# Optimization experiments

Hardware: AMD Instinct MI355X
Metric: run time of the kernel (lower is better)

Reference implementation:

```python
import jax, jax.numpy as jnp
import numpy as np

KS = 7            # kernel_size
DIL = 1           # dilatation
H = 96
W = 96
PAD = DIL * (KS - 1) // 2
SHIFTS = [s * DIL for s in range(KS)]


def stack_kernel(a, axis=-2):
    # a: [B, H+2*PAD, W+2*PAD, C] -> [B, H, W, ks^2, C] (or stacked on `axis`)
    return jnp.stack([a[:, y:H + y, x:W + x] for y in SHIFTS for x in SHIFTS], axis=axis)


def make_padding_mask():
    # zeros inside, -inf in the halo; stacked per window position -> [1,H,W,ks^2]
    z = jnp.pad(jnp.zeros((1, H, W, 1), jnp.float32),
                ((0, 0), (PAD, PAD), (PAD, PAD), (0, 0)),
                constant_values=-jnp.inf)
    return stack_kernel(z, axis=-1)[..., 0, :]  # [1,H,W,ks^2]


def setup_inputs() -> dict:
    key = jax.random.key(0)
    ks = jax.random.split(key, 8)
    B, C, KD, OD = 2, 128, 64, 128
    Q = jax.random.normal(ks[0], (B, H, W, C), jnp.float32)
    K = jax.random.normal(ks[1], (B, H, W, C), jnp.float32)
    V = jax.random.normal(ks[2], (B, H, W, C), jnp.float32)
    s = 1.0 / np.sqrt(C)
    Wq = jax.random.normal(ks[3], (C, KD), jnp.float32) * s
    Wk = jax.random.normal(ks[4], (C, KD), jnp.float32) * s
    Wv = jax.random.normal(ks[5], (C, OD), jnp.float32) * s
    return {"Q": Q, "K": K, "V": V,
            "Wq": Wq, "bq": jnp.zeros((KD,), jnp.float32),
            "Wk": Wk, "bk": jnp.zeros((KD,), jnp.float32),
            "Wv": Wv, "bv": jnp.zeros((OD,), jnp.float32)}


def reference(Q, K, V, Wq, bq, Wk, bk, Wv, bv):
    # Dense projections (key_dim is not None)
    q = Q @ Wq + bq                      # [B,H,W,KD]
    k = K @ Wk + bk                      # [B,H,W,KD]
    Dk = jnp.asarray(q.shape[-1], q.dtype)

    pad4 = ((0, 0), (PAD, PAD), (PAD, PAD), (0, 0))
    k_stk = stack_kernel(jnp.pad(k, pad4), axis=-2)   # [B,H,W,ks^2,KD]
    mask = make_padding_mask()                        # [1,H,W,ks^2]

    # w = Q . K_neighbors + padding mask; softmax over ks^2 window
    w = jnp.einsum('bhwd,bhwkd->bhwk', q, k_stk) + mask
    scores = jax.nn.softmax(w / jnp.sqrt(Dk), axis=-1)  # [B,H,W,ks^2]

    v_stk = stack_kernel(jnp.pad(V, pad4), axis=-2)   # [B,H,W,ks^2,E]
    out = jnp.einsum('bhwk,bhwke->bhwe', scores, v_stk)
    # V_d Dense with relu (out_dim is not None)
    out = jax.nn.relu(out @ Wv + bv)                  # [B,H,W,out_dim]
    return out
```

## Files before the change

### kernel.cpp

```cpp
#include <hip/hip_runtime.h>
#include <math.h>

#define BH 2
#define HH 96
#define WW 96
#define CC 128
#define NPIX (BH*HH*WW)

#define TH 8
#define TW 4
#define NH 140
#define NHP 160

#define NEGBIG (-3.0e38f)

typedef __attribute__((ext_vector_type(8))) short short8;
typedef __attribute__((ext_vector_type(4))) float f32x4;

__device__ __forceinline__ unsigned short f2bf(float f) {
    union { float f; unsigned u; } a; a.f = f;
    return (unsigned short)((a.u + 0x7FFFu + ((a.u >> 16) & 1u)) >> 16);
}
__device__ __forceinline__ unsigned packbf(float x, float y) {
    return (unsigned)f2bf(x) | ((unsigned)f2bf(y) << 16);
}

__global__ __launch_bounds__(256) void prep_proj_kernel(
    const float* __restrict__ Qg, const float* __restrict__ Kg,
    const float* __restrict__ V,  const float* __restrict__ Wq,
    const float* __restrict__ bq, const float* __restrict__ Wk,
    const float* __restrict__ bk, const float* __restrict__ Wv,
    unsigned short* __restrict__ q_bf, unsigned short* __restrict__ k_bf,
    unsigned short* __restrict__ v_bf, unsigned short* __restrict__ WvT)
{
    const int bid = blockIdx.x;
    const int tid = threadIdx.x;

    if (bid < 576) {
        const int lane = tid & 63;
        const int wvv  = tid >> 6;
        const int gw   = bid * 4 + wvv;
        const bool isq = gw < 1152;
        const int row0 = (isq ? gw : gw - 1152) * 16;

        const float* __restrict__ X   = isq ? Qg : Kg;
        const float* __restrict__ Wt  = isq ? Wq : Wk;
        const float* __restrict__ bia = isq ? bq : bk;
        unsigned short* __restrict__ Y = isq ? q_bf : k_bf;

        const int qd = lane >> 4, m = lane & 15;

        short8 afr[4];
        #pragma unroll
        for (int ks = 0; ks < 4; ++ks) {
            const float4* __restrict__ src = reinterpret_cast<const float4*>(
                X + (size_t)(row0 + m) * 128 + ks * 32 + qd * 8);
            const float4 a0 = src[0], a1 = src[1];
            short8 f;
            f[0] = (short)f2bf(a0.x); f[1] = (short)f2bf(a0.y);
            f[2] = (short)f2bf(a0.z); f[3] = (short)f2bf(a0.w);
            f[4] = (short)f2bf(a1.x); f[5] = (short)f2bf(a1.y);
            f[6] = (short)f2bf(a1.z); f[7] = (short)f2bf(a1.w);
            afr[ks] = f;
        }

        #pragma unroll
        for (int n = 0; n < 4; ++n) {
            f32x4 acc = {};
            #pragma unroll
            for (int ks = 0; ks < 4; ++ks) {
                short8 bfr;
                #pragma unroll
                for (int j = 0; j < 8; ++j)
                    bfr[j] = (short)f2bf(Wt[(ks * 32 + qd * 8 + j) * 64 + n * 16 + m]);
                acc = __builtin_amdgcn_mfma_f32_16x16x32_bf16(afr[ks], bfr, acc, 0, 0, 0);
            }
            const int col = n * 16 + m;
            const float bb = bia[col];
            #pragma unroll
            for (int r = 0; r < 4; ++r)
                Y[(size_t)(row0 + qd * 4 + r) * 64 + col] = f2bf(acc[r] + bb);
        }
    } else if (bid < 1728) {
        const int idx = (bid - 576) * 256 + tid;
        const float4* __restrict__ V4 = reinterpret_cast<const float4*>(V);
        const float4 a = V4[idx * 2], b = V4[idx * 2 + 1];
        uint4 o;
        o.x = packbf(a.x, a.y); o.y = packbf(a.z, a.w);
        o.z = packbf(b.x, b.y); o.w = packbf(b.z, b.w);
        reinterpret_cast<uint4*>(v_bf)[idx] = o;
    } else {
        const int base = (bid - 1728) * 1024 + tid * 4;
        #pragma unroll
        for (int i = 0; i < 4; ++i) {
            const int e = base + i;
            WvT[e] = f2bf(Wv[(e & 127) * 128 + (e >> 7)]);
        }
    }
}

#define PS_OFF 0
#define PS_STRIDE 168
#define AS_OFF 5376
#define AS_STRIDE 136
#define SM_OFF 9728
#define OFF_OFF 9984
#define LDS_N 10304

__global__ __launch_bounds__(256) void attn_kernel(
    const unsigned short* __restrict__ q_bf, const unsigned short* __restrict__ k_bf,
    const unsigned short* __restrict__ v_bf, const unsigned short* __restrict__ WvT,
    const float* __restrict__ bv, float* __restrict__ out)
{
    __shared__ unsigned short lds[LDS_N];
    const int tid  = threadIdx.x;
    const int lane = tid & 63;
    const int wv   = tid >> 6;
    const int mt   = wv & 1;
    const int ng   = wv >> 1;

    const int bid  = blockIdx.x;
    const int bimg = bid / 288;
    const int tidx = bid % 288;
    const int ty = tidx / 24, tx = tidx % 24;
    const int y0 = ty * TH, x0 = tx * TW;

    const int qd = lane >> 4, m = lane & 15;

    int* __restrict__ offsI = reinterpret_cast<int*>(&lds[OFF_OFF]);
    float* __restrict__ smf = reinterpret_cast<float*>(&lds[SM_OFF]);

    if (tid < NHP) {
        const int r = tid;
        const int hy = (r * 6554) >> 16;
        const int hx = r - hy * 10;
        const int iy = y0 - 3 + hy, ix = x0 - 3 + hx;
        int o = -1;
        if (((unsigned)iy < HH) & ((unsigned)ix < WW) & (r < NH))
            o = (bimg * HH + iy) * WW + ix;
        offsI[r] = o;
    }
    __syncthreads();

    short8 qa[2];
    {
        const int p  = mt * 16 + m;
        const int py = p >> 2, px = p & 3;
        const size_t gq = (size_t)(bimg * HH + y0 + py) * WW + (x0 + px);
        #pragma unroll
        for (int ks = 0; ks < 2; ++ks)
            qa[ks] = *reinterpret_cast<const short8*>(q_bf + gq * 64 + ks * 32 + qd * 8);
    }

    f32x4 sc[5];
    int offh[5];
    #pragma unroll
    for (int n5 = 0; n5 < 5; ++n5) {
        const int nt = ng * 5 + n5;
        const int oh = offsI[nt * 16 + m];
        offh[n5] = oh;
        const size_t ob = (size_t)(oh < 0 ? 0 : oh) * 64;
        f32x4 a = {};
        #pragma unroll
        for (int ks = 0; ks < 2; ++ks) {
            const short8 bfr = *reinterpret_cast<const short8*>(k_bf + ob + ks * 32 + qd * 8);
            a = __builtin_amdgcn_mfma_f32_16x16x32_bf16(qa[ks], bfr, a, 0, 0, 0);
        }
        sc[n5] = a;
    }

    float mx[4] = {NEGBIG, NEGBIG, NEGBIG, NEGBIG};
    #pragma unroll
    for (int n5 = 0; n5 < 5; ++n5) {
        const int h  = (ng * 5 + n5) * 16 + m;
        const int hy = (h * 6554) >> 16;
        const int hx = h - hy * 10;
        const bool imgok = offh[n5] >= 0;
        #pragma unroll
        for (int r = 0; r < 4; ++r) {
            const int p  = mt * 16 + qd * 4 + r;
            const int py = p >> 2, px = p & 3;
            const bool ok = imgok & ((unsigned)(hy - py) <= 6u) & ((unsigned)(hx - px) <= 6u);
            const float s = ok ? sc[n5][r] * 0.125f : NEGBIG;
            sc[n5][r] = s;
            mx[r] = fmaxf(mx[r], s);
        }
    }
    #pragma unroll
    for (int r = 0; r < 4; ++r)
        #pragma unroll
        for (int off = 1; off < 16; off <<= 1)
            mx[r] = fmaxf(mx[r], __shfl_xor(mx[r], off));

    float sm[4] = {0.f, 0.f, 0.f, 0.f};
    #pragma unroll
    for (int n5 = 0; n5 < 5; ++n5)
        #pragma unroll
        for (int r = 0; r < 4; ++r) {
            const float s = sc[n5][r];
            const float e = (s > -1.0e38f) ? __expf(s - mx[r]) : 0.f;
            sc[n5][r] = e;
            sm[r] += e;
        }
    #pragma unroll
    for (int r = 0; r < 4; ++r)
        #pragma unroll
        for (int off = 1; off < 16; off <<= 1)
            sm[r] += __shfl_xor(sm[r], off);

    if (m == 0) {
        #pragma unroll
        for (int r = 0; r < 4; ++r) {
            const int row = mt * 16 + qd * 4 + r;
            smf[row * 2 + ng]      = mx[r];
            smf[64 + row * 2 + ng] = sm[r];
        }
    }
    __syncthreads();

    float fac[4];
    #pragma unroll
    for (int r = 0; r < 4; ++r) {
        const int row = mt * 16 + qd * 4 + r;
        const float m0 = smf[row * 2 + 0];
        const float m1 = smf[row * 2 + 1];
        const float M  = fmaxf(m0, m1);
        const float s0 = smf[64 + row * 2 + 0];
        const float s1 = smf[64 + row * 2 + 1];
        const float S  = s0 * __expf(m0 - M) + s1 * __expf(m1 - M);
        fac[r] = __expf(mx[r] - M) / S;
    }

    #pragma unroll
    for (int n5 = 0; n5 < 5; ++n5)
        #pragma unroll
        for (int r = 0; r < 4; ++r) {
            const int row = mt * 16 + qd * 4 + r;
            const int col = (ng * 5 + n5) * 16 + m;
            lds[PS_OFF + row * PS_STRIDE + col] = f2bf(sc[n5][r] * fac[r]);
        }
    __syncthreads();

    short8 pa[5];
    #pragma unroll
    for (int ks = 0; ks < 5; ++ks)
        pa[ks] = *reinterpret_cast<const short8*>(
            &lds[PS_OFF + (mt * 16 + m) * PS_STRIDE + ks * 32 + qd * 8]);

    f32x4 oacc[4] = {};
    #pragma unroll
    for (int ks = 0; ks < 5; ++ks) {
        const unsigned short* vbase[8];
        #pragma unroll
        for (int j = 0; j < 8; ++j) {
            const int o = offsI[ks * 32 + qd * 8 + j];
            vbase[j] = v_bf + (size_t)(o < 0 ? 0 : o) * 128;
        }
        #pragma unroll
        for (int n4 = 0; n4 < 4; ++n4) {
            const int ch = (ng * 4 + n4) * 16 + m;
            short8 bfr;
            #pragma unroll
            for (int j = 0; j < 8; ++j)
                bfr[j] = (short)vbase[j][ch];
            oacc[n4] = __builtin_amdgcn_mfma_f32_16x16x32_bf16(pa[ks], bfr, oacc[n4], 0, 0, 0);
        }
    }

    #pragma unroll
    for (int n4 = 0; n4 < 4; ++n4)
        #pragma unroll
        for (int r = 0; r < 4; ++r) {
            const int row = mt * 16 + qd * 4 + r;
            const int col = (ng * 4 + n4) * 16 + m;
            lds[AS_OFF + row * AS_STRIDE + col] = f2bf(oacc[n4][r]);
        }
    __syncthreads();

    short8 aa[4];
    #pragma unroll
    for (int ks = 0; ks < 4; ++ks)
        aa[ks] = *reinterpret_cast<const short8*>(
            &lds[AS_OFF + (mt * 16 + m) * AS_STRIDE + ks * 32 + qd * 8]);

    #pragma unroll
    for (int n4 = 0; n4 < 4; ++n4) {
        const int nt = ng * 4 + n4;
        f32x4 a = {};
        #pragma unroll
        for (int ks = 0; ks < 4; ++ks) {
            const short8 bfr = *reinterpret_cast<const short8*>(
                WvT + (nt * 16 + m) * 128 + ks * 32 + qd * 8);
            a = __builtin_amdgcn_mfma_f32_16x16x32_bf16(aa[ks], bfr, a, 0, 0, 0);
        }
        const int col = nt * 16 + m;
        const float bb = bv[col];
        #pragma unroll
        for (int r = 0; r < 4; ++r) {
            const int p  = mt * 16 + qd * 4 + r;
            const int py = p >> 2, px = p & 3;
            const size_t gp = (size_t)(bimg * HH + y0 + py) * WW + (x0 + px);
            out[gp * 128 + col] = fmaxf(a[r] + bb, 0.f);
        }
    }
}

extern "C" void kernel_launch(void* const* d_in, const int* in_sizes, int n_in,
                              void* d_out, int out_size, void* d_ws, size_t ws_size,
                              hipStream_t stream)
{
    const float* Q  = (const float*)d_in[0];
    const float* K  = (const float*)d_in[1];
    const float* V  = (const float*)d_in[2];
    const float* Wq = (const float*)d_in[3];
    const float* bq = (const float*)d_in[4];
    const float* Wk = (const float*)d_in[5];
    const float* bk = (const float*)d_in[6];
    const float* Wv = (const float*)d_in[7];
    const float* bv = (const float*)d_in[8];
    float* out = (float*)d_out;

    unsigned short* WvT  = (unsigned short*)d_ws;
    unsigned short* q_bf = WvT + 16384;
    unsigned short* k_bf = q_bf + (size_t)NPIX * 64;
    unsigned short* v_bf = k_bf + (size_t)NPIX * 64;

    prep_proj_kernel<<<1744, 256, 0, stream>>>(Q, K, V, Wq, bq, Wk, bk, Wv,
                                               q_bf, k_bf, v_bf, WvT);
    attn_kernel<<<576, 256, 0, stream>>>(q_bf, k_bf, v_bf, WvT, bv, out);
}
```

Measured before the change: 110.8 us.

## Stage V halo in LDS from fp32, pre-transpose weights, drop V bf16 pass

Removes the separate V-to-bf16 conversion pass. The attention kernel now loads the fp32 V halo tile straight from global memory into LDS, converting and swizzling it there, so the PV MFMA operands are gathered from LDS instead of scattered global loads. Weight transposition to bf16 moves into a small kernel so the projection kernel does vector loads of pre-transposed weights. Each wave also computes all ten score tiles itself, which removes the cross-wave softmax reduction and one barrier at the price of duplicated QK MFMAs. The trade-offs are an extra kernel launch and larger LDS use, which may lower occupancy.

```diff
diff --git a/kernel.cpp b/kernel.cpp
--- a/kernel.cpp
+++ b/kernel.cpp
@@ -4,7 +4,6 @@
 #define BH 2
 #define HH 96
 #define WW 96
-#define CC 128
 #define NPIX (BH*HH*WW)
 
 #define TH 8
@@ -25,91 +24,79 @@
     return (unsigned)f2bf(x) | ((unsigned)f2bf(y) << 16);
 }
 
-__global__ __launch_bounds__(256) void prep_proj_kernel(
+__global__ __launch_bounds__(256) void wprep_kernel(
+    const float* __restrict__ Wq, const float* __restrict__ Wk,
+    const float* __restrict__ Wv, unsigned short* __restrict__ wbase)
+{
+    const int e = blockIdx.x * 256 + threadIdx.x;
+    if (e < 8192)       { wbase[e] = f2bf(Wq[(e & 127) * 64 + (e >> 7)]); }
+    else if (e < 16384) { const int t = e - 8192;
+                          wbase[e] = f2bf(Wk[(t & 127) * 64 + (t >> 7)]); }
+    else                { const int t = e - 16384;
+                          wbase[e] = f2bf(Wv[(t & 127) * 128 + (t >> 7)]); }
+}
+
+__global__ __launch_bounds__(256) void proj_kernel(
     const float* __restrict__ Qg, const float* __restrict__ Kg,
-    const float* __restrict__ V,  const float* __restrict__ Wq,
-    const float* __restrict__ bq, const float* __restrict__ Wk,
-    const float* __restrict__ bk, const float* __restrict__ Wv,
-    unsigned short* __restrict__ q_bf, unsigned short* __restrict__ k_bf,
-    unsigned short* __restrict__ v_bf, unsigned short* __restrict__ WvT)
-{
-    const int bid = blockIdx.x;
-    const int tid = threadIdx.x;
-
-    if (bid < 576) {
-        const int lane = tid & 63;
-        const int wvv  = tid >> 6;
-        const int gw   = bid * 4 + wvv;
-        const bool isq = gw < 1152;
-        const int row0 = (isq ? gw : gw - 1152) * 16;
-
-        const float* __restrict__ X   = isq ? Qg : Kg;
-        const float* __restrict__ Wt  = isq ? Wq : Wk;
-        const float* __restrict__ bia = isq ? bq : bk;
-        unsigned short* __restrict__ Y = isq ? q_bf : k_bf;
-
-        const int qd = lane >> 4, m = lane & 15;
-
-        short8 afr[4];
+    const unsigned short* __restrict__ wbase,
+    const float* __restrict__ bq, const float* __restrict__ bk,
+    unsigned short* __restrict__ q_bf, unsigned short* __restrict__ k_bf)
+{
+    const int tid  = threadIdx.x;
+    const int lane = tid & 63;
+    const int wvv  = tid >> 6;
+    const int gw   = blockIdx.x * 4 + wvv;
+    const bool isq = gw < 1152;
+    const int row0 = (isq ? gw : gw - 1152) * 16;
+
+    const float* __restrict__ X = isq ? Qg : Kg;
+    const unsigned short* __restrict__ WT = isq ? wbase : (wbase + 8192);
+    const float* __restrict__ bia = isq ? bq : bk;
+    unsigned short* __restrict__ Y = isq ? q_bf : k_bf;
+
+    const int qd = lane >> 4, m = lane & 15;
+
+    short8 afr[4];
+    #pragma unroll
+    for (int ks = 0; ks < 4; ++ks) {
+        const float4* __restrict__ src = reinterpret_cast<const float4*>(
+            X + (size_t)(row0 + m) * 128 + ks * 32 + qd * 8);
+        const float4 a0 = src[0], a1 = src[1];
+        short8 f;
+        f[0] = (short)f2bf(a0.x); f[1] = (short)f2bf(a0.y);
+        f[2] = (short)f2bf(a0.z); f[3] = (short)f2bf(a0.w);
+        f[4] = (short)f2bf(a1.x); f[5] = (short)f2bf(a1.y);
+        f[6] = (short)f2bf(a1.z); f[7] = (short)f2bf(a1.w);
+        afr[ks] = f;
+    }
+
+    #pragma unroll
+    for (int n = 0; n < 4; ++n) {
+        f32x4 acc = {};
         #pragma unroll
         for (int ks = 0; ks < 4; ++ks) {
-            const float4* __restrict__ src = reinterpret_cast<const float4*>(
-                X + (size_t)(row0 + m) * 128 + ks * 32 + qd * 8);
-            const float4 a0 = src[0], a1 = src[1];
-            short8 f;
-            f[0] = (short)f2bf(a0.x); f[1] = (short)f2bf(a0.y);
-            f[2] = (short)f2bf(a0.z); f[3] = (short)f2bf(a0.w);
-            f[4] = (short)f2bf(a1.x); f[5] = (short)f2bf(a1.y);
-            f[6] = (short)f2bf(a1.z); f[7] = (short)f2bf(a1.w);
-            afr[ks] = f;
-        }
-
-        #pragma unroll
-        for (int n = 0; n < 4; ++n) {
-            f32x4 acc = {};
-            #pragma unroll
-            for (int ks = 0; ks < 4; ++ks) {
-                short8 bfr;
-                #pragma unroll
-                for (int j = 0; j < 8; ++j)
-                    bfr[j] = (short)f2bf(Wt[(ks * 32 + qd * 8 + j) * 64 + n * 16 + m]);
-                acc = __builtin_amdgcn_mfma_f32_16x16x32_bf16(afr[ks], bfr, acc, 0, 0, 0);
-            }
-            const int col = n * 16 + m;
-            const float bb = bia[col];
-            #pragma unroll
-            for (int r = 0; r < 4; ++r)
-                Y[(size_t)(row0 + qd * 4 + r) * 64 + col] = f2bf(acc[r] + bb);
-        }
-    } else if (bid < 1728) {
-        const int idx = (bid - 576) * 256 + tid;
-        const float4* __restrict__ V4 = reinterpret_cast<const float4*>(V);
-        const float4 a = V4[idx * 2], b = V4[idx * 2 + 1];
-        uint4 o;
-        o.x = packbf(a.x, a.y); o.y = packbf(a.z, a.w);
-        o.z = packbf(b.x, b.y); o.w = packbf(b.z, b.w);
-        reinterpret_cast<uint4*>(v_bf)[idx] = o;
-    } else {
-        const int base = (bid - 1728) * 1024 + tid * 4;
-        #pragma unroll
-        for (int i = 0; i < 4; ++i) {
-            const int e = base + i;
-            WvT[e] = f2bf(Wv[(e & 127) * 128 + (e >> 7)]);
-        }
-    }
-}
-
-#define PS_OFF 0
+            const short8 bfr = *reinterpret_cast<const short8*>(
+                WT + (n * 16 + m) * 128 + ks * 32 + qd * 8);
+            acc = __builtin_amdgcn_mfma_f32_16x16x32_bf16(afr[ks], bfr, acc, 0, 0, 0);
+        }
+        const int col = n * 16 + m;
+        const float bb = bia[col];
+        #pragma unroll
+        for (int r = 0; r < 4; ++r)
+            Y[(size_t)(row0 + qd * 4 + r) * 64 + col] = f2bf(acc[r] + bb);
+    }
+}
+
+#define VS_OFF 0
+#define PS_OFF 20480
 #define PS_STRIDE 168
-#define AS_OFF 5376
+#define AS_OFF 25856
 #define AS_STRIDE 136
-#define SM_OFF 9728
-#define OFF_OFF 9984
-#define LDS_N 10304
+#define LDS_N 30208
 
 __global__ __launch_bounds__(256) void attn_kernel(
     const unsigned short* __restrict__ q_bf, const unsigned short* __restrict__ k_bf,
-    const unsigned short* __restrict__ v_bf, const unsigned short* __restrict__ WvT,
+    const float* __restrict__ V, const unsigned short* __restrict__ WvT,
     const float* __restrict__ bv, float* __restrict__ out)
 {
     __shared__ unsigned short lds[LDS_N];
@@ -127,20 +114,22 @@
 
     const int qd = lane >> 4, m = lane & 15;
 
-    int* __restrict__ offsI = reinterpret_cast<int*>(&lds[OFF_OFF]);
-    float* __restrict__ smf = reinterpret_cast<float*>(&lds[SM_OFF]);
-
-    if (tid < NHP) {
-        const int r = tid;
-        const int hy = (r * 6554) >> 16;
-        const int hx = r - hy * 10;
-        const int iy = y0 - 3 + hy, ix = x0 - 3 + hx;
-        int o = -1;
-        if (((unsigned)iy < HH) & ((unsigned)ix < WW) & (r < NH))
-            o = (bimg * HH + iy) * WW + ix;
-        offsI[r] = o;
-    }
-    __syncthreads();
+    {
+        unsigned* __restrict__ vsu = reinterpret_cast<unsigned*>(lds);
+        #pragma unroll 8
+        for (int i = 0; i < 40; ++i) {
+            const int r  = i * 4 + wv;
+            const int hy = (r * 6554) >> 16;
+            const int hx = r - hy * 10;
+            const int iy = y0 - 3 + hy, ix = x0 - 3 + hx;
+            const bool ok = ((unsigned)iy < HH) & ((unsigned)ix < WW) & (r < NH);
+            float2 v = make_float2(0.f, 0.f);
+            if (ok)
+                v = *reinterpret_cast<const float2*>(
+                    V + (size_t)((bimg * HH + iy) * WW + ix) * 128 + lane * 2);
+            vsu[r * 64 + ((lane + ((r >> 3) & 3) * 8) & 63)] = packbf(v.x, v.y);
+        }
+    }
 
     short8 qa[2];
     {
@@ -152,37 +141,39 @@
             qa[ks] = *reinterpret_cast<const short8*>(q_bf + gq * 64 + ks * 32 + qd * 8);
     }
 
-    f32x4 sc[5];
-    int offh[5];
-    #pragma unroll
-    for (int n5 = 0; n5 < 5; ++n5) {
-        const int nt = ng * 5 + n5;
-        const int oh = offsI[nt * 16 + m];
-        offh[n5] = oh;
-        const size_t ob = (size_t)(oh < 0 ? 0 : oh) * 64;
+    f32x4 sc[10];
+    #pragma unroll
+    for (int nt = 0; nt < 10; ++nt) {
+        const int h  = nt * 16 + m;
+        const int hy = (h * 6554) >> 16;
+        const int hx = h - hy * 10;
+        const int iy = y0 - 3 + hy, ix = x0 - 3 + hx;
+        const bool ok = ((unsigned)iy < HH) & ((unsigned)ix < WW) & (h < NH);
+        const size_t ob = ok ? (size_t)((bimg * HH + iy) * WW + ix) * 64 : 0;
         f32x4 a = {};
         #pragma unroll
         for (int ks = 0; ks < 2; ++ks) {
             const short8 bfr = *reinterpret_cast<const short8*>(k_bf + ob + ks * 32 + qd * 8);
             a = __builtin_amdgcn_mfma_f32_16x16x32_bf16(qa[ks], bfr, a, 0, 0, 0);
         }
-        sc[n5] = a;
+        sc[nt] = a;
     }
 
     float mx[4] = {NEGBIG, NEGBIG, NEGBIG, NEGBIG};
     #pragma unroll
-    for (int n5 = 0; n5 < 5; ++n5) {
-        const int h  = (ng * 5 + n5) * 16 + m;
+    for (int nt = 0; nt < 10; ++nt) {
+        const int h  = nt * 16 + m;
         const int hy = (h * 6554) >> 16;
         const int hx = h - hy * 10;
-        const bool imgok = offh[n5] >= 0;
+        const int iy = y0 - 3 + hy, ix = x0 - 3 + hx;
+        const bool imgok = ((unsigned)iy < HH) & ((unsigned)ix < WW) & (h < NH);
         #pragma unroll
         for (int r = 0; r < 4; ++r) {
             const int p  = mt * 16 + qd * 4 + r;
             const int py = p >> 2, px = p & 3;
             const bool ok = imgok & ((unsigned)(hy - py) <= 6u) & ((unsigned)(hx - px) <= 6u);
-            const float s = ok ? sc[n5][r] * 0.125f : NEGBIG;
-            sc[n5][r] = s;
+            const float s = ok ? sc[nt][r] * 0.125f : NEGBIG;
+            sc[nt][r] = s;
             mx[r] = fmaxf(mx[r], s);
         }
     }
@@ -194,51 +185,31 @@
 
     float sm[4] = {0.f, 0.f, 0.f, 0.f};
     #pragma unroll
-    for (int n5 = 0; n5 < 5; ++n5)
-        #pragma unroll
-        for (int r = 0; r < 4; ++r) {
-            const float s = sc[n5][r];
+    for (int nt = 0; nt < 10; ++nt)
+        #pragma unroll
+        for (int r = 0; r < 4; ++r) {
+            const float s = sc[nt][r];
             const float e = (s > -1.0e38f) ? __expf(s - mx[r]) : 0.f;
-            sc[n5][r] = e;
+            sc[nt][r] = e;
             sm[r] += e;
         }
     #pragma unroll
-    for (int r = 0; r < 4; ++r)
+    for (int r = 0; r < 4; ++r) {
         #pragma unroll
         for (int off = 1; off < 16; off <<= 1)
             sm[r] += __shfl_xor(sm[r], off);
-
-    if (m == 0) {
+        sm[r] = 1.0f / sm[r];
+    }
+
+    #pragma unroll
+    for (int n5 = 0; n5 < 5; ++n5) {
+        const int nt = ng * 5 + n5;
         #pragma unroll
         for (int r = 0; r < 4; ++r) {
             const int row = mt * 16 + qd * 4 + r;
-            smf[row * 2 + ng]      = mx[r];
-            smf[64 + row * 2 + ng] = sm[r];
-        }
-    }
-    __syncthreads();
-
-    float fac[4];
-    #pragma unroll
-    for (int r = 0; r < 4; ++r) {
-        const int row = mt * 16 + qd * 4 + r;
-        const float m0 = smf[row * 2 + 0];
-        const float m1 = smf[row * 2 + 1];
-        const float M  = fmaxf(m0, m1);
-        const float s0 = smf[64 + row * 2 + 0];
-        const float s1 = smf[64 + row * 2 + 1];
-        const float S  = s0 * __expf(m0 - M) + s1 * __expf(m1 - M);
-        fac[r] = __expf(mx[r] - M) / S;
-    }
-
-    #pragma unroll
-    for (int n5 = 0; n5 < 5; ++n5)
-        #pragma unroll
-        for (int r = 0; r < 4; ++r) {
-            const int row = mt * 16 + qd * 4 + r;
-            const int col = (ng * 5 + n5) * 16 + m;
-            lds[PS_OFF + row * PS_STRIDE + col] = f2bf(sc[n5][r] * fac[r]);
-        }
+            lds[PS_OFF + row * PS_STRIDE + nt * 16 + m] = f2bf(sc[nt][r] * sm[r]);
+        }
+    }
     __syncthreads();
 
     short8 pa[5];
@@ -250,19 +221,14 @@
     f32x4 oacc[4] = {};
     #pragma unroll
     for (int ks = 0; ks < 5; ++ks) {
-        const unsigned short* vbase[8];
-        #pragma unroll
-        for (int j = 0; j < 8; ++j) {
-            const int o = offsI[ks * 32 + qd * 8 + j];
-            vbase[j] = v_bf + (size_t)(o < 0 ? 0 : o) * 128;
-        }
+        const int kbase = ks * 32 + qd * 8;
         #pragma unroll
         for (int n4 = 0; n4 < 4; ++n4) {
-            const int ch = (ng * 4 + n4) * 16 + m;
+            const int colp = (((ng * 4 + n4) * 16 + m) + qd * 16) & 127;
             short8 bfr;
             #pragma unroll
             for (int j = 0; j < 8; ++j)
-                bfr[j] = (short)vbase[j][ch];
+                bfr[j] = (short)lds[VS_OFF + (kbase + j) * 128 + colp];
             oacc[n4] = __builtin_amdgcn_mfma_f32_16x16x32_bf16(pa[ks], bfr, oacc[n4], 0, 0, 0);
         }
     }
@@ -320,12 +286,12 @@
     const float* bv = (const float*)d_in[8];
     float* out = (float*)d_out;
 
-    unsigned short* WvT  = (unsigned short*)d_ws;
-    unsigned short* q_bf = WvT + 16384;
-    unsigned short* k_bf = q_bf + (size_t)NPIX * 64;
-    unsigned short* v_bf = k_bf + (size_t)NPIX * 64;
-
-    prep_proj_kernel<<<1744, 256, 0, stream>>>(Q, K, V, Wq, bq, Wk, bk, Wv,
-                                               q_bf, k_bf, v_bf, WvT);
-    attn_kernel<<<576, 256, 0, stream>>>(q_bf, k_bf, v_bf, WvT, bv, out);
-}
+    unsigned short* wbase = (unsigned short*)d_ws;
+    unsigned short* WvT   = wbase + 16384;
+    unsigned short* q_bf  = wbase + 32768;
+    unsigned short* k_bf  = q_bf + (size_t)NPIX * 64;
+
+    wprep_kernel<<<128, 256, 0, stream>>>(Wq, Wk, Wv, wbase);
+    proj_kernel<<<576, 256, 0, stream>>>(Q, K, wbase, bq, bk, q_bf, k_bf);
+    attn_kernel<<<576, 256, 0, stream>>>(q_bf, k_bf, V, WvT, bv, out);
+}
```

Measured after the change: 138.4 us. 25.0% more time.

## Shrink attention tile to 4x4 pixels with per-wave full-window softmax

Applied to the files above, without the earlier changes.

Halves the attention tile from 8x4 to 4x4 pixels, so the halo is 100 entries and the grid doubles to 1152 blocks. Each wave now computes all seven score tiles for its 16 pixels, finishing the softmax locally. This drops the cross-wave max/sum merge through shared memory and one barrier. The trade-off is redundant QK MFMA work across waves and a larger halo-to-pixel ratio, so each output pixel pulls more K/V gather traffic.

```diff
diff --git a/kernel.cpp b/kernel.cpp
--- a/kernel.cpp
+++ b/kernel.cpp
@@ -4,13 +4,11 @@
 #define BH 2
 #define HH 96
 #define WW 96
-#define CC 128
 #define NPIX (BH*HH*WW)
 
-#define TH 8
+#define TH 4
 #define TW 4
-#define NH 140
-#define NHP 160
+#define NH 100
 
 #define NEGBIG (-3.0e38f)
 
@@ -100,12 +98,11 @@
 }
 
 #define PS_OFF 0
-#define PS_STRIDE 168
-#define AS_OFF 5376
+#define PS_STRIDE 136
+#define AS_OFF 2176
 #define AS_STRIDE 136
-#define SM_OFF 9728
-#define OFF_OFF 9984
-#define LDS_N 10304
+#define OFF_OFF 4352
+#define LDS_N 4608
 
 __global__ __launch_bounds__(256) void attn_kernel(
     const unsigned short* __restrict__ q_bf, const unsigned short* __restrict__ k_bf,
@@ -116,73 +113,68 @@
     const int tid  = threadIdx.x;
     const int lane = tid & 63;
     const int wv   = tid >> 6;
-    const int mt   = wv & 1;
-    const int ng   = wv >> 1;
 
     const int bid  = blockIdx.x;
-    const int bimg = bid / 288;
-    const int tidx = bid % 288;
+    const int bimg = bid / 576;
+    const int tidx = bid % 576;
     const int ty = tidx / 24, tx = tidx % 24;
     const int y0 = ty * TH, x0 = tx * TW;
 
     const int qd = lane >> 4, m = lane & 15;
 
     int* __restrict__ offsI = reinterpret_cast<int*>(&lds[OFF_OFF]);
-    float* __restrict__ smf = reinterpret_cast<float*>(&lds[SM_OFF]);
-
-    if (tid < NHP) {
+
+    if (tid < 128) {
         const int r = tid;
         const int hy = (r * 6554) >> 16;
         const int hx = r - hy * 10;
         const int iy = y0 - 3 + hy, ix = x0 - 3 + hx;
-        int o = -1;
+        int o = 0;
         if (((unsigned)iy < HH) & ((unsigned)ix < WW) & (r < NH))
             o = (bimg * HH + iy) * WW + ix;
         offsI[r] = o;
     }
-    __syncthreads();
 
     short8 qa[2];
     {
-        const int p  = mt * 16 + m;
-        const int py = p >> 2, px = p & 3;
+        const int py = m >> 2, px = m & 3;
         const size_t gq = (size_t)(bimg * HH + y0 + py) * WW + (x0 + px);
         #pragma unroll
         for (int ks = 0; ks < 2; ++ks)
             qa[ks] = *reinterpret_cast<const short8*>(q_bf + gq * 64 + ks * 32 + qd * 8);
     }
 
-    f32x4 sc[5];
-    int offh[5];
-    #pragma unroll
-    for (int n5 = 0; n5 < 5; ++n5) {
-        const int nt = ng * 5 + n5;
-        const int oh = offsI[nt * 16 + m];
-        offh[n5] = oh;
-        const size_t ob = (size_t)(oh < 0 ? 0 : oh) * 64;
+    f32x4 sc[7];
+    #pragma unroll
+    for (int nt = 0; nt < 7; ++nt) {
+        const int h  = nt * 16 + m;
+        const int hy = (h * 6554) >> 16;
+        const int hx = h - hy * 10;
+        const int iy = y0 - 3 + hy, ix = x0 - 3 + hx;
+        const bool ok = ((unsigned)iy < HH) & ((unsigned)ix < WW) & (h < NH);
+        const size_t ob = ok ? (size_t)((bimg * HH + iy) * WW + ix) * 64 : 0;
         f32x4 a = {};
         #pragma unroll
         for (int ks = 0; ks < 2; ++ks) {
             const short8 bfr = *reinterpret_cast<const short8*>(k_bf + ob + ks * 32 + qd * 8);
             a = __builtin_amdgcn_mfma_f32_16x16x32_bf16(qa[ks], bfr, a, 0, 0, 0);
         }
-        sc[n5] = a;
+        sc[nt] = a;
     }
 
     float mx[4] = {NEGBIG, NEGBIG, NEGBIG, NEGBIG};
     #pragma unroll
-    for (int n5 = 0; n5 < 5; ++n5) {
-        const int h  = (ng * 5 + n5) * 16 + m;
+    for (int nt = 0; nt < 7; ++nt) {
+        const int h  = nt * 16 + m;
         const int hy = (h * 6554) >> 16;
         const int hx = h - hy * 10;
-        const bool imgok = offh[n5] >= 0;
+        const int iy = y0 - 3 + hy, ix = x0 - 3 + hx;
+        const bool imgok = ((unsigned)iy < HH) & ((unsigned)ix < WW) & (h < NH);
         #pragma unroll
         for (int r = 0; r < 4; ++r) {
-            const int p  = mt * 16 + qd * 4 + r;
-            const int py = p >> 2, px = p & 3;
-            const bool ok = imgok & ((unsigned)(hy - py) <= 6u) & ((unsigned)(hx - px) <= 6u);
-            const float s = ok ? sc[n5][r] * 0.125f : NEGBIG;
-            sc[n5][r] = s;
+            const bool ok = imgok & ((unsigned)(hy - qd) <= 6u) & ((unsigned)(hx - r) <= 6u);
+            const float s = ok ? sc[nt][r] * 0.125f : NEGBIG;
+            sc[nt][r] = s;
             mx[r] = fmaxf(mx[r], s);
         }
     }
@@ -194,98 +186,80 @@
 
     float sm[4] = {0.f, 0.f, 0.f, 0.f};
     #pragma unroll
-    for (int n5 = 0; n5 < 5; ++n5)
+    for (int nt = 0; nt < 7; ++nt)
         #pragma unroll
         for (int r = 0; r < 4; ++r) {
-            const float s = sc[n5][r];
+            const float s = sc[nt][r];
             const float e = (s > -1.0e38f) ? __expf(s - mx[r]) : 0.f;
-            sc[n5][r] = e;
+            sc[nt][r] = e;
             sm[r] += e;
         }
     #pragma unroll
-    for (int r = 0; r < 4; ++r)
+    for (int r = 0; r < 4; ++r) {
         #pragma unroll
         for (int off = 1; off < 16; off <<= 1)
             sm[r] += __shfl_xor(sm[r], off);
-
-    if (m == 0) {
-        #pragma unroll
-        for (int r = 0; r < 4; ++r) {
-            const int row = mt * 16 + qd * 4 + r;
-            smf[row * 2 + ng]      = mx[r];
-            smf[64 + row * 2 + ng] = sm[r];
-        }
+        sm[r] = 1.0f / sm[r];
+    }
+
+    #pragma unroll
+    for (int nt = 0; nt < 7; ++nt) {
+        if ((nt >> 1) == wv) {
+            #pragma unroll
+            for (int r = 0; r < 4; ++r)
+                lds[PS_OFF + (qd * 4 + r) * PS_STRIDE + nt * 16 + m] =
+                    f2bf(sc[nt][r] * sm[r]);
+        }
+    }
+    if (wv == 3) {
+        #pragma unroll
+        for (int r = 0; r < 4; ++r)
+            lds[PS_OFF + (qd * 4 + r) * PS_STRIDE + 112 + m] = 0;
     }
     __syncthreads();
 
-    float fac[4];
-    #pragma unroll
-    for (int r = 0; r < 4; ++r) {
-        const int row = mt * 16 + qd * 4 + r;
-        const float m0 = smf[row * 2 + 0];
-        const float m1 = smf[row * 2 + 1];
-        const float M  = fmaxf(m0, m1);
-        const float s0 = smf[64 + row * 2 + 0];
-        const float s1 = smf[64 + row * 2 + 1];
-        const float S  = s0 * __expf(m0 - M) + s1 * __expf(m1 - M);
-        fac[r] = __expf(mx[r] - M) / S;
-    }
-
-    #pragma unroll
-    for (int n5 = 0; n5 < 5; ++n5)
-        #pragma unroll
-        for (int r = 0; r < 4; ++r) {
-            const int row = mt * 16 + qd * 4 + r;
-            const int col = (ng * 5 + n5) * 16 + m;
-            lds[PS_OFF + row * PS_STRIDE + col] = f2bf(sc[n5][r] * fac[r]);
-        }
-    __syncthreads();
-
-    short8 pa[5];
-    #pragma unroll
-    for (int ks = 0; ks < 5; ++ks)
+    short8 pa[4];
+    #pragma unroll
+    for (int ks = 0; ks < 4; ++ks)
         pa[ks] = *reinterpret_cast<const short8*>(
-            &lds[PS_OFF + (mt * 16 + m) * PS_STRIDE + ks * 32 + qd * 8]);
-
-    f32x4 oacc[4] = {};
-    #pragma unroll
-    for (int ks = 0; ks < 5; ++ks) {
-        const unsigned short* vbase[8];
-        #pragma unroll
-        for (int j = 0; j < 8; ++j) {
-            const int o = offsI[ks * 32 + qd * 8 + j];
-            vbase[j] = v_bf + (size_t)(o < 0 ? 0 : o) * 128;
-        }
-        #pragma unroll
-        for (int n4 = 0; n4 < 4; ++n4) {
-            const int ch = (ng * 4 + n4) * 16 + m;
+            &lds[PS_OFF + m * PS_STRIDE + ks * 32 + qd * 8]);
+
+    f32x4 oacc[2] = {};
+    #pragma unroll
+    for (int ks = 0; ks < 4; ++ks) {
+        const int kbase = ks * 32 + qd * 8;
+        const unsigned short* vb[8];
+        #pragma unroll
+        for (int j = 0; j < 8; ++j)
+            vb[j] = v_bf + (size_t)offsI[kbase + j] * 128;
+        #pragma unroll
+        for (int n2 = 0; n2 < 2; ++n2) {
+            const int ch = (wv * 2 + n2) * 16 + m;
             short8 bfr;
             #pragma unroll
             for (int j = 0; j < 8; ++j)
-                bfr[j] = (short)vbase[j][ch];
-            oacc[n4] = __builtin_amdgcn_mfma_f32_16x16x32_bf16(pa[ks], bfr, oacc[n4], 0, 0, 0);
-        }
-    }
-
-    #pragma unroll
-    for (int n4 = 0; n4 < 4; ++n4)
-        #pragma unroll
-        for (int r = 0; r < 4; ++r) {
-            const int row = mt * 16 + qd * 4 + r;
-            const int col = (ng * 4 + n4) * 16 + m;
-            lds[AS_OFF + row * AS_STRIDE + col] = f2bf(oacc[n4][r]);
-        }
+                bfr[j] = (short)vb[j][ch];
+            oacc[n2] = __builtin_amdgcn_mfma_f32_16x16x32_bf16(pa[ks], bfr, oacc[n2], 0, 0, 0);
+        }
+    }
+
+    #pragma unroll
+    for (int n2 = 0; n2 < 2; ++n2)
+        #pragma unroll
+        for (int r = 0; r < 4; ++r)
+            lds[AS_OFF + (qd * 4 + r) * AS_STRIDE + (wv * 2 + n2) * 16 + m] =
+                f2bf(oacc[n2][r]);
     __syncthreads();
 
     short8 aa[4];
     #pragma unroll
     for (int ks = 0; ks < 4; ++ks)
         aa[ks] = *reinterpret_cast<const short8*>(
-            &lds[AS_OFF + (mt * 16 + m) * AS_STRIDE + ks * 32 + qd * 8]);
-
-    #pragma unroll
-    for (int n4 = 0; n4 < 4; ++n4) {
-        const int nt = ng * 4 + n4;
+            &lds[AS_OFF + m * AS_STRIDE + ks * 32 + qd * 8]);
+
+    #pragma unroll
+    for (int n2 = 0; n2 < 2; ++n2) {
+        const int nt = wv * 2 + n2;
         f32x4 a = {};
         #pragma unroll
         for (int ks = 0; ks < 4; ++ks) {
@@ -297,8 +271,7 @@
         const float bb = bv[col];
         #pragma unroll
         for (int r = 0; r < 4; ++r) {
-            const int p  = mt * 16 + qd * 4 + r;
-            const int py = p >> 2, px = p & 3;
+            const int py = qd, px = r;
             const size_t gp = (size_t)(bimg * HH + y0 + py) * WW + (x0 + px);
             out[gp * 128 + col] = fmaxf(a[r] + bb, 0.f);
         }
@@ -320,12 +293,13 @@
     const float* bv = (const float*)d_in[8];
     float* out = (float*)d_out;
 
-    unsigned short* WvT  = (unsigned short*)d_ws;
-    unsigned short* q_bf = WvT + 16384;
-    unsigned short* k_bf = q_bf + (size_t)NPIX * 64;
-    unsigned short* v_bf = k_bf + (size_t)NPIX * 64;
+    unsigned short* wbase = (unsigned short*)d_ws;
+    unsigned short* WvT   = wbase + 16384;
+    unsigned short* q_bf  = wbase + 32768;
+    unsigned short* k_bf  = q_bf + (size_t)NPIX * 64;
+    unsigned short* v_bf  = k_bf + (size_t)NPIX * 64;
 
     prep_proj_kernel<<<1744, 256, 0, stream>>>(Q, K, V, Wq, bq, Wk, bk, Wv,
                                                q_bf, k_bf, v_bf, WvT);
-    attn_kernel<<<576, 256, 0, stream>>>(q_bf, k_bf, v_bf, WvT, bv, out);
-}
+    attn_kernel<<<1152, 256, 0, stream>>>(q_bf, k_bf, v_bf, WvT, bv, out);
+}
```

Result: slower. 114.0 us (+2.9%).

## Stage projection weights in LDS and split attention across eight waves

Applied to the files above, without the earlier changes.

The projection kernel now transposes and converts each Wq/Wk matrix to bf16 once per block in shared memory, replacing the per-lane strided global loads and conversions. The attention kernel doubles its block to 512 threads so eight waves share the score tiles (3/3/2/2 split) and the value and output channels, with the softmax reduction widened to four partial groups. Halo offsets for the scores are computed inline rather than read from LDS, which removes one barrier. The trade-off is a larger block, more cross-wave reduction, and uneven tile counts per wave.

```diff
diff --git a/kernel.cpp b/kernel.cpp
--- a/kernel.cpp
+++ b/kernel.cpp
@@ -4,7 +4,6 @@
 #define BH 2
 #define HH 96
 #define WW 96
-#define CC 128
 #define NPIX (BH*HH*WW)
 
 #define TH 8
@@ -24,6 +23,8 @@
 __device__ __forceinline__ unsigned packbf(float x, float y) {
     return (unsigned)f2bf(x) | ((unsigned)f2bf(y) << 16);
 }
+
+#define WT_STRIDE 136
 
 __global__ __launch_bounds__(256) void prep_proj_kernel(
     const float* __restrict__ Qg, const float* __restrict__ Kg,
@@ -33,21 +34,36 @@
     unsigned short* __restrict__ q_bf, unsigned short* __restrict__ k_bf,
     unsigned short* __restrict__ v_bf, unsigned short* __restrict__ WvT)
 {
+    __shared__ unsigned short WT[64 * WT_STRIDE];
     const int bid = blockIdx.x;
     const int tid = threadIdx.x;
 
     if (bid < 576) {
-        const int lane = tid & 63;
-        const int wvv  = tid >> 6;
-        const int gw   = bid * 4 + wvv;
-        const bool isq = gw < 1152;
-        const int row0 = (isq ? gw : gw - 1152) * 16;
-
+        const bool isq = bid < 288;
         const float* __restrict__ X   = isq ? Qg : Kg;
         const float* __restrict__ Wt  = isq ? Wq : Wk;
         const float* __restrict__ bia = isq ? bq : bk;
         unsigned short* __restrict__ Y = isq ? q_bf : k_bf;
 
+        {
+            const float4* __restrict__ W4 = reinterpret_cast<const float4*>(Wt);
+            #pragma unroll
+            for (int i = 0; i < 8; ++i) {
+                const int e  = tid + 256 * i;
+                const int k  = e >> 4;
+                const int n4 = (e & 15) * 4;
+                const float4 v = W4[e];
+                WT[(n4 + 0) * WT_STRIDE + k] = f2bf(v.x);
+                WT[(n4 + 1) * WT_STRIDE + k] = f2bf(v.y);
+                WT[(n4 + 2) * WT_STRIDE + k] = f2bf(v.z);
+                WT[(n4 + 3) * WT_STRIDE + k] = f2bf(v.w);
+            }
+        }
+        __syncthreads();
+
+        const int lane = tid & 63;
+        const int wvv  = tid >> 6;
+        const int row0 = ((bid % 288) * 4 + wvv) * 16;
         const int qd = lane >> 4, m = lane & 15;
 
         short8 afr[4];
@@ -69,10 +85,8 @@
             f32x4 acc = {};
             #pragma unroll
             for (int ks = 0; ks < 4; ++ks) {
-                short8 bfr;
-                #pragma unroll
-                for (int j = 0; j < 8; ++j)
-                    bfr[j] = (short)f2bf(Wt[(ks * 32 + qd * 8 + j) * 64 + n * 16 + m]);
+                const short8 bfr = *reinterpret_cast<const short8*>(
+                    &WT[(n * 16 + m) * WT_STRIDE + ks * 32 + qd * 8]);
                 acc = __builtin_amdgcn_mfma_f32_16x16x32_bf16(afr[ks], bfr, acc, 0, 0, 0);
             }
             const int col = n * 16 + m;
@@ -104,10 +118,10 @@
 #define AS_OFF 5376
 #define AS_STRIDE 136
 #define SM_OFF 9728
-#define OFF_OFF 9984
-#define LDS_N 10304
-
-__global__ __launch_bounds__(256) void attn_kernel(
+#define OFF_OFF 10240
+#define LDS_N 10560
+
+__global__ __launch_bounds__(512) void attn_kernel(
     const unsigned short* __restrict__ q_bf, const unsigned short* __restrict__ k_bf,
     const unsigned short* __restrict__ v_bf, const unsigned short* __restrict__ WvT,
     const float* __restrict__ bv, float* __restrict__ out)
@@ -127,8 +141,8 @@
 
     const int qd = lane >> 4, m = lane & 15;
 
-    int* __restrict__ offsI = reinterpret_cast<int*>(&lds[OFF_OFF]);
-    float* __restrict__ smf = reinterpret_cast<float*>(&lds[SM_OFF]);
+    int*   __restrict__ offsI = reinterpret_cast<int*>(&lds[OFF_OFF]);
+    float* __restrict__ smf   = reinterpret_cast<float*>(&lds[SM_OFF]);
 
     if (tid < NHP) {
         const int r = tid;
@@ -140,26 +154,29 @@
             o = (bimg * HH + iy) * WW + ix;
         offsI[r] = o;
     }
-    __syncthreads();
 
     short8 qa[2];
     {
-        const int p  = mt * 16 + m;
-        const int py = p >> 2, px = p & 3;
+        const int py = mt * 4 + (m >> 2), px = m & 3;
         const size_t gq = (size_t)(bimg * HH + y0 + py) * WW + (x0 + px);
         #pragma unroll
         for (int ks = 0; ks < 2; ++ks)
             qa[ks] = *reinterpret_cast<const short8*>(q_bf + gq * 64 + ks * 32 + qd * 8);
     }
 
-    f32x4 sc[5];
-    int offh[5];
-    #pragma unroll
-    for (int n5 = 0; n5 < 5; ++n5) {
-        const int nt = ng * 5 + n5;
-        const int oh = offsI[nt * 16 + m];
-        offh[n5] = oh;
-        const size_t ob = (size_t)(oh < 0 ? 0 : oh) * 64;
+    const int ntbase = (ng < 2) ? ng * 3 : 6 + (ng - 2) * 2;
+    const int ntcnt  = (ng < 2) ? 3 : 2;
+
+    f32x4 sc[3];
+    #pragma unroll
+    for (int n5 = 0; n5 < 3; ++n5) {
+        if (n5 >= ntcnt) break;
+        const int h  = (ntbase + n5) * 16 + m;
+        const int hy = (h * 6554) >> 16;
+        const int hx = h - hy * 10;
+        const int iy = y0 - 3 + hy, ix = x0 - 3 + hx;
+        const bool ok = ((unsigned)iy < HH) & ((unsigned)ix < WW) & (h < NH);
+        const size_t ob = ok ? (size_t)((bimg * HH + iy) * WW + ix) * 64 : 0;
         f32x4 a = {};
         #pragma unroll
         for (int ks = 0; ks < 2; ++ks) {
@@ -171,16 +188,17 @@
 
     float mx[4] = {NEGBIG, NEGBIG, NEGBIG, NEGBIG};
     #pragma unroll
-    for (int n5 = 0; n5 < 5; ++n5) {
-        const int h  = (ng * 5 + n5) * 16 + m;
+    for (int n5 = 0; n5 < 3; ++n5) {
+        if (n5 >= ntcnt) break;
+        const int h  = (ntbase + n5) * 16 + m;
         const int hy = (h * 6554) >> 16;
         const int hx = h - hy * 10;
-        const bool imgok = offh[n5] >= 0;
-        #pragma unroll
-        for (int r = 0; r < 4; ++r) {
-            const int p  = mt * 16 + qd * 4 + r;
-            const int py = p >> 2, px = p & 3;
-            const bool ok = imgok & ((unsigned)(hy - py) <= 6u) & ((unsigned)(hx - px) <= 6u);
+        const int iy = y0 - 3 + hy, ix = x0 - 3 + hx;
+        const bool imgok = ((unsigned)iy < HH) & ((unsigned)ix < WW) & (h < NH);
+        const int py = mt * 4 + qd;
+        #pragma unroll
+        for (int r = 0; r < 4; ++r) {
+            const bool ok = imgok & ((unsigned)(hy - py) <= 6u) & ((unsigned)(hx - r) <= 6u);
             const float s = ok ? sc[n5][r] * 0.125f : NEGBIG;
             sc[n5][r] = s;
             mx[r] = fmaxf(mx[r], s);
@@ -194,7 +212,8 @@
 
     float sm[4] = {0.f, 0.f, 0.f, 0.f};
     #pragma unroll
-    for (int n5 = 0; n5 < 5; ++n5)
+    for (int n5 = 0; n5 < 3; ++n5) {
+        if (n5 >= ntcnt) break;
         #pragma unroll
         for (int r = 0; r < 4; ++r) {
             const float s = sc[n5][r];
@@ -202,6 +221,7 @@
             sc[n5][r] = e;
             sm[r] += e;
         }
+    }
     #pragma unroll
     for (int r = 0; r < 4; ++r)
         #pragma unroll
@@ -212,8 +232,8 @@
         #pragma unroll
         for (int r = 0; r < 4; ++r) {
             const int row = mt * 16 + qd * 4 + r;
-            smf[row * 2 + ng]      = mx[r];
-            smf[64 + row * 2 + ng] = sm[r];
+            smf[row * 4 + ng]       = mx[r];
+            smf[128 + row * 4 + ng] = sm[r];
         }
     }
     __syncthreads();
@@ -222,23 +242,31 @@
     #pragma unroll
     for (int r = 0; r < 4; ++r) {
         const int row = mt * 16 + qd * 4 + r;
-        const float m0 = smf[row * 2 + 0];
-        const float m1 = smf[row * 2 + 1];
-        const float M  = fmaxf(m0, m1);
-        const float s0 = smf[64 + row * 2 + 0];
-        const float s1 = smf[64 + row * 2 + 1];
-        const float S  = s0 * __expf(m0 - M) + s1 * __expf(m1 - M);
-        fac[r] = __expf(mx[r] - M) / S;
-    }
-
-    #pragma unroll
-    for (int n5 = 0; n5 < 5; ++n5)
+        float M = smf[row * 4 + 0];
+        M = fmaxf(M, smf[row * 4 + 1]);
+        M = fmaxf(M, smf[row * 4 + 2]);
+        M = fmaxf(M, smf[row * 4 + 3]);
+        float S = 0.f;
+        #pragma unroll
+        for (int g = 0; g < 4; ++g) {
+            const float mg = smf[row * 4 + g];
+            const float eg = (mg > -1.0e38f) ? __expf(mg - M) : 0.f;
+            S += smf[128 + row * 4 + g] * eg;
+        }
+        const float eo = (mx[r] > -1.0e38f) ? __expf(mx[r] - M) : 0.f;
+        fac[r] = eo / S;
+    }
+
+    #pragma unroll
+    for (int n5 = 0; n5 < 3; ++n5) {
+        if (n5 >= ntcnt) break;
         #pragma unroll
         for (int r = 0; r < 4; ++r) {
             const int row = mt * 16 + qd * 4 + r;
-            const int col = (ng * 5 + n5) * 16 + m;
+            const int col = (ntbase + n5) * 16 + m;
             lds[PS_OFF + row * PS_STRIDE + col] = f2bf(sc[n5][r] * fac[r]);
         }
+    }
     __syncthreads();
 
     short8 pa[5];
@@ -247,33 +275,34 @@
         pa[ks] = *reinterpret_cast<const short8*>(
             &lds[PS_OFF + (mt * 16 + m) * PS_STRIDE + ks * 32 + qd * 8]);
 
-    f32x4 oacc[4] = {};
+    f32x4 oacc[2] = {};
     #pragma unroll
     for (int ks = 0; ks < 5; ++ks) {
-        const unsigned short* vbase[8];
+        const int kbase = ks * 32 + qd * 8;
+        const unsigned short* vb[8];
         #pragma unroll
         for (int j = 0; j < 8; ++j) {
-            const int o = offsI[ks * 32 + qd * 8 + j];
-            vbase[j] = v_bf + (size_t)(o < 0 ? 0 : o) * 128;
-        }
-        #pragma unroll
-        for (int n4 = 0; n4 < 4; ++n4) {
-            const int ch = (ng * 4 + n4) * 16 + m;
+            const int o = offsI[kbase + j];
+            vb[j] = v_bf + (size_t)(o < 0 ? 0 : o) * 128;
+        }
+        #pragma unroll
+        for (int n2 = 0; n2 < 2; ++n2) {
+            const int ch = (ng * 2 + n2) * 16 + m;
             short8 bfr;
             #pragma unroll
             for (int j = 0; j < 8; ++j)
-                bfr[j] = (short)vbase[j][ch];
-            oacc[n4] = __builtin_amdgcn_mfma_f32_16x16x32_bf16(pa[ks], bfr, oacc[n4], 0, 0, 0);
-        }
-    }
-
-    #pragma unroll
-    for (int n4 = 0; n4 < 4; ++n4)
+                bfr[j] = (short)vb[j][ch];
+            oacc[n2] = __builtin_amdgcn_mfma_f32_16x16x32_bf16(pa[ks], bfr, oacc[n2], 0, 0, 0);
+        }
+    }
+
+    #pragma unroll
+    for (int n2 = 0; n2 < 2; ++n2)
         #pragma unroll
         for (int r = 0; r < 4; ++r) {
             const int row = mt * 16 + qd * 4 + r;
-            const int col = (ng * 4 + n4) * 16 + m;
-            lds[AS_OFF + row * AS_STRIDE + col] = f2bf(oacc[n4][r]);
+            const int col = (ng * 2 + n2) * 16 + m;
+            lds[AS_OFF + row * AS_STRIDE + col] = f2bf(oacc[n2][r]);
         }
     __syncthreads();
 
@@ -284,8 +313,8 @@
             &lds[AS_OFF + (mt * 16 + m) * AS_STRIDE + ks * 32 + qd * 8]);
 
     #pragma unroll
-    for (int n4 = 0; n4 < 4; ++n4) {
-        const int nt = ng * 4 + n4;
+    for (int n2 = 0; n2 < 2; ++n2) {
+        const int nt = ng * 2 + n2;
         f32x4 a = {};
         #pragma unroll
         for (int ks = 0; ks < 4; ++ks) {
@@ -297,8 +326,7 @@
         const float bb = bv[col];
         #pragma unroll
         for (int r = 0; r < 4; ++r) {
-            const int p  = mt * 16 + qd * 4 + r;
-            const int py = p >> 2, px = p & 3;
+            const int py = mt * 4 + qd, px = r;
             const size_t gp = (size_t)(bimg * HH + y0 + py) * WW + (x0 + px);
             out[gp * 128 + col] = fmaxf(a[r] + bb, 0.f);
         }
@@ -320,12 +348,13 @@
     const float* bv = (const float*)d_in[8];
     float* out = (float*)d_out;
 
-    unsigned short* WvT  = (unsigned short*)d_ws;
-    unsigned short* q_bf = WvT + 16384;
-    unsigned short* k_bf = q_bf + (size_t)NPIX * 64;
-    unsigned short* v_bf = k_bf + (size_t)NPIX * 64;
+    unsigned short* wbase = (unsigned short*)d_ws;
+    unsigned short* WvT   = wbase + 16384;
+    unsigned short* q_bf  = wbase + 32768;
+    unsigned short* k_bf  = q_bf + (size_t)NPIX * 64;
+    unsigned short* v_bf  = k_bf + (size_t)NPIX * 64;
 
     prep_proj_kernel<<<1744, 256, 0, stream>>>(Q, K, V, Wq, bq, Wk, bk, Wv,
                                                q_bf, k_bf, v_bf, WvT);
-    attn_kernel<<<576, 256, 0, stream>>>(q_bf, k_bf, v_bf, WvT, bv, out);
-}
+    attn_kernel<<<576, 512, 0, stream>>>(q_bf, k_bf, v_bf, WvT, bv, out);
+}
```

New measurement: 109.9 us. No clear change (-0.8%).
